# Performance work log

Hardware: AMD Instinct MI355X
Metric: run time of the kernel (lower is better)

The kernel has to match this reference:

```python
import jax, jax.numpy as jnp
import numpy as np

Q = 3
MAX_SHIFT = 4.0


def setup_inputs() -> dict:
    key = jax.random.key(0)
    k1, k2, k3, k4 = jax.random.split(key, 4)
    x = jax.random.normal(k1, (16, 64, 128, 128), jnp.float32)
    weight = jax.random.normal(k2, (64, 192, 3, 3), jnp.float32) * 0.05
    bias = jax.random.normal(k3, (64,), jnp.float32) * 0.05
    # shift_init='random': uniform in [-1, 1]; forward multiplies by max_shift
    shifts = jax.random.uniform(k4, (64, 2), jnp.float32, -1.0, 1.0)
    return {"x": x, "weight": weight, "bias": bias, "shifts": shifts}


def _shift_bilinear(x, shifts, max_shift):
    """Per-channel bilinear translation, matching affine_grid+grid_sample
    (align_corners=False, padding_mode='zeros').
    x: [N,C,H,W]; shifts: [C,2] with (sx, sy) in normalized units.
    Sample location for output (i,j) is (i + sy*max_shift, j + sx*max_shift)."""
    N, C, H, W = x.shape
    sx = shifts[:, 0] * max_shift  # pixels along width
    sy = shifts[:, 1] * max_shift  # pixels along height
    ys = jnp.arange(H, dtype=x.dtype)[None, :] + sy[:, None]  # [C,H]
    xs = jnp.arange(W, dtype=x.dtype)[None, :] + sx[:, None]  # [C,W]
    y0f = jnp.floor(ys); fy = ys - y0f; y0 = y0f.astype(jnp.int32); y1 = y0 + 1
    x0f = jnp.floor(xs); fx = xs - x0f; x0 = x0f.astype(jnp.int32); x1 = x0 + 1

    def gather(yi, xi):
        vy = (yi >= 0) & (yi < H)          # [C,H]
        vx = (xi >= 0) & (xi < W)          # [C,W]
        yc = jnp.clip(yi, 0, H - 1)
        xc = jnp.clip(xi, 0, W - 1)
        g = jnp.take_along_axis(x, yc[None, :, :, None], axis=2)
        g = jnp.take_along_axis(g, xc[None, :, None, :], axis=3)
        m = (vy[:, :, None] & vx[:, None, :]).astype(x.dtype)[None]
        return g * m

    w00 = ((1 - fy)[:, :, None] * (1 - fx)[:, None, :])[None]
    w01 = ((1 - fy)[:, :, None] * fx[:, None, :])[None]
    w10 = (fy[:, :, None] * (1 - fx)[:, None, :])[None]
    w11 = (fy[:, :, None] * fx[:, None, :])[None]
    return (w00 * gather(y0, x0) + w01 * gather(y0, x1)
            + w10 * gather(y1, x0) + w11 * gather(y1, x1))


def reference(x, weight, bias, shifts):
    # 1) per-channel learnless shift (grid_sample bilinear, zeros padding)
    xs = _shift_bilinear(x, shifts, MAX_SHIFT)
    # 2) Maclaurin power series: concat(x, x^2, ..., x^q) on channels -> [N, C*q, H, W]
    xq = jnp.concatenate([xs ** i for i in range(1, Q + 1)], axis=1)
    # 3) dense conv (groups=1), stride 1, padding 1
    out = jax.lax.conv_general_dilated(
        xq, weight, window_strides=(1, 1), padding=((1, 1), (1, 1)),
        dimension_numbers=("NCHW", "OIHW", "NCHW"))
    return out + bias[None, :, None, None]
```

## Files before the change

kernel.cpp:

```cpp
#include <hip/hip_runtime.h>
#include <hip/hip_bf16.h>
#include <math.h>

#define NB 16
#define C_IN 64
#define C_OUT 64
#define HH 128
#define WW 128
#define MAX_SHIFT 4.0f

typedef __attribute__((ext_vector_type(8))) short bf16x8;
typedef __attribute__((ext_vector_type(4))) float f32x4;
typedef __attribute__((ext_vector_type(4))) unsigned int u32x4;

__device__ inline unsigned short bf16_rne(float f) {
    unsigned u = __builtin_bit_cast(unsigned, f);
    u += 0x7fffu + ((u >> 16) & 1u);
    return (unsigned short)(u >> 16);
}
__device__ inline unsigned pack_bf16x2(float lo, float hi) {
    unsigned ul = __builtin_bit_cast(unsigned, lo);
    unsigned uh = __builtin_bit_cast(unsigned, hi);
    ul += 0x7fffu + ((ul >> 16) & 1u);
    uh += 0x7fffu + ((uh >> 16) & 1u);
    return (ul >> 16) | (uh & 0xffff0000u);
}

#define CPAD 66

__global__ __launch_bounds__(256)
void shift_v(const float* __restrict__ x, const float* __restrict__ shifts,
             unsigned short* __restrict__ xv) {
    __shared__ unsigned short row[64 * CPAD];
    __shared__ float s_fx[C_IN], s_fy[C_IN];
    __shared__ int s_dx[C_IN], s_dy[C_IN];

    int b = blockIdx.x;
    int wh = b & 1;
    int h  = (b >> 1) & 127;
    int n  = b >> 8;
    int tid = threadIdx.x;
    int wv = tid >> 6;
    int l  = tid & 63;

    if (tid < C_IN) {
        float sx = shifts[2 * tid] * MAX_SHIFT;
        float sy = shifts[2 * tid + 1] * MAX_SHIFT;
        float fx0 = floorf(sx), fy0 = floorf(sy);
        s_dx[tid] = (int)fx0; s_dy[tid] = (int)fy0;
        s_fx[tid] = sx - fx0;  s_fy[tid] = sy - fy0;
    }
    __syncthreads();

    const float* xn = x + (size_t)n * (C_IN * HH * WW);
    int w = wh * 64 + l;
    unsigned short* rw = row + l * CPAD;

    #pragma unroll 4
    for (int it = 0; it < 16; ++it) {
        int c = it * 4 + wv;
        int dx = s_dx[c], dy = s_dy[c];
        float fx = s_fx[c], fy = s_fy[c];
        const float* xp = xn + (size_t)c * (HH * WW);
        int y0 = h + dy, y1 = y0 + 1;
        bool vy0 = ((unsigned)y0 < (unsigned)HH);
        bool vy1 = ((unsigned)y1 < (unsigned)HH);
        const float* r0 = xp + y0 * WW;
        const float* r1 = xp + y1 * WW;

        int x0 = w + dx, x1 = x0 + 1;
        bool vx0 = ((unsigned)x0 < (unsigned)WW);
        bool vx1 = ((unsigned)x1 < (unsigned)WW);
        float v00 = (vy0 && vx0) ? r0[x0] : 0.f;
        float v01 = (vy0 && vx1) ? r0[x1] : 0.f;
        float v10 = (vy1 && vx0) ? r1[x0] : 0.f;
        float v11 = (vy1 && vx1) ? r1[x1] : 0.f;
        float v = (1.f - fy) * ((1.f - fx) * v00 + fx * v01)
                + fy * ((1.f - fx) * v10 + fx * v11);
        rw[c] = bf16_rne(v);
    }
    __syncthreads();

    const unsigned* rp = (const unsigned*)row;
    unsigned* dst = (unsigned*)xv + ((size_t)((n * HH + h) * WW) + wh * 64) * 32;
    #pragma unroll
    for (int itw = 0; itw < 8; ++itw) {
        int o32 = itw * 256 + tid;
        int wl = o32 >> 5;
        int c4 = o32 & 31;
        dst[o32] = rp[wl * (CPAD / 2) + c4];
    }
}

__global__ void prep_w3(const float* __restrict__ w, unsigned short* __restrict__ wbuf) {
    int id = blockIdx.x * 256 + threadIdx.x;
    int e = id & 7;
    int l = (id >> 3) & 63;
    int f = id >> 9;
    int mf = f & 3;
    int f2 = f >> 2;
    int kb = f2 % 6;
    int t  = f2 / 6;
    int cg = kb / 3;
    int p  = kb - cg * 3;
    int cl = (l >> 4) * 8 + e;
    int co = mf * 16 + (l & 15);
    wbuf[id] = bf16_rne(w[(co * 192 + p * 64 + cg * 32 + cl) * 9 + t]);
}

__global__ __launch_bounds__(256, 2)
void conv2d(const unsigned short* __restrict__ xv,
            const unsigned short* __restrict__ wbuf,
            const float* __restrict__ bias,
            float* __restrict__ out) {
    __shared__ unsigned short tile[324 * 44];

    int bid = blockIdx.x;
    int wg = (bid & 7) * 128 + (bid >> 3);
    int n  = wg >> 6;
    int t6 = wg & 63;
    int i0 = (t6 >> 3) * 16;
    int j0 = (t6 & 7) * 16;

    int tid = threadIdx.x;
    int l  = tid & 63;
    int wv = tid >> 6;
    int lm = l & 15;
    int lg = l >> 4;

    f32x4 acc[4][4];
    #pragma unroll
    for (int mf = 0; mf < 4; ++mf) {
        #pragma unroll
        for (int r = 0; r < 4; ++r) {
            float bv = bias[mf * 16 + lg * 4 + r];
            #pragma unroll
            for (int nf = 0; nf < 4; ++nf) acc[mf][nf][r] = bv;
        }
    }

    const unsigned short* xn = xv + (size_t)n * (HH * WW * 64);

    #pragma unroll 1
    for (int kb = 0; kb < 6; ++kb) {
        int cg = kb / 3;
        int p  = kb - cg * 3;
        __syncthreads();
        #pragma unroll
        for (int it = 0; it < 6; ++it) {
            int item = it * 256 + tid;
            if (item < 1296) {
                int px = item >> 2, sub = item & 3;
                int rr = px / 18;
                int cc = px - rr * 18;
                int gi = i0 - 1 + rr, gj = j0 - 1 + cc;
                u32x4 dv = {0, 0, 0, 0};
                if ((unsigned)gi < (unsigned)HH && (unsigned)gj < (unsigned)WW)
                    dv = *(const u32x4*)(xn + ((size_t)gi * WW + gj) * 64 + cg * 32 + sub * 8);
                u32x4 ov;
                if (p == 0) {
                    ov = dv;
                } else {
                    #pragma unroll
                    for (int q = 0; q < 4; ++q) {
                        unsigned u = dv[q];
                        float f0 = __builtin_bit_cast(float, u << 16);
                        float f1 = __builtin_bit_cast(float, u & 0xffff0000u);
                        float r0 = f0 * f0, r1 = f1 * f1;
                        if (p == 2) { r0 *= f0; r1 *= f1; }
                        ov[q] = pack_bf16x2(r0, r1);
                    }
                }
                *(u32x4*)((char*)tile + px * 88 + sub * 16) = ov;
            }
        }
        __syncthreads();

        bf16x8 Af[4];
        #pragma unroll
        for (int mf = 0; mf < 4; ++mf)
            Af[mf] = *(const bf16x8*)(wbuf + (size_t)((0 * 6 + kb) * 4 + mf) * 512 + l * 8);

        #pragma unroll 1
        for (int t = 0; t < 9; ++t) {
            bf16x8 Afn[4];
            int tn = (t < 8) ? t + 1 : t;
            #pragma unroll
            for (int mf = 0; mf < 4; ++mf)
                Afn[mf] = *(const bf16x8*)(wbuf + (size_t)((tn * 6 + kb) * 4 + mf) * 512 + l * 8);

            int ky = t / 3, kx = t - ky * 3;
            #pragma unroll
            for (int nf = 0; nf < 4; ++nf) {
                int off = ((wv * 4 + nf + ky) * 18 + (lm + kx)) * 88 + lg * 16;
                bf16x8 bfrag = *(const bf16x8*)((const char*)tile + off);
                #pragma unroll
                for (int mf = 0; mf < 4; ++mf)
                    acc[mf][nf] = __builtin_amdgcn_mfma_f32_16x16x32_bf16(Af[mf], bfrag, acc[mf][nf], 0, 0, 0);
            }
            #pragma unroll
            for (int mf = 0; mf < 4; ++mf) Af[mf] = Afn[mf];
        }
    }

    #pragma unroll
    for (int mf = 0; mf < 4; ++mf) {
        #pragma unroll
        for (int nf = 0; nf < 4; ++nf) {
            int rowi = i0 + wv * 4 + nf;
            int col = j0 + lm;
            #pragma unroll
            for (int r = 0; r < 4; ++r) {
                int co = mf * 16 + lg * 4 + r;
                out[(((size_t)n * C_OUT + co) * HH + rowi) * WW + col] = acc[mf][nf][r];
            }
        }
    }
}

#define S_PX 100

__global__ __launch_bounds__(256, 2)
void conv_f(const float* __restrict__ x,
            const float* __restrict__ shifts,
            const unsigned short* __restrict__ wbuf,
            const float* __restrict__ bias,
            float* __restrict__ out) {
    __shared__ unsigned short tile[324 * S_PX];
    __shared__ float s_fx[C_IN], s_fy[C_IN];
    __shared__ int s_dx[C_IN], s_dy[C_IN];

    int bid = blockIdx.x;
    int wg = (bid & 7) * 128 + (bid >> 3);
    int n  = wg >> 6;
    int t6 = wg & 63;
    int i0 = (t6 >> 3) * 16;
    int j0 = (t6 & 7) * 16;

    int tid = threadIdx.x;
    int l  = tid & 63;
    int wv = tid >> 6;
    int lm = l & 15;
    int lg = l >> 4;

    if (tid < C_IN) {
        float sx = shifts[2 * tid] * MAX_SHIFT;
        float sy = shifts[2 * tid + 1] * MAX_SHIFT;
        float fx0 = floorf(sx), fy0 = floorf(sy);
        s_dx[tid] = (int)fx0; s_dy[tid] = (int)fy0;
        s_fx[tid] = sx - fx0;  s_fy[tid] = sy - fy0;
    }

    f32x4 acc[4][4];
    #pragma unroll
    for (int mf = 0; mf < 4; ++mf) {
        #pragma unroll
        for (int r = 0; r < 4; ++r) {
            float bv = bias[mf * 16 + lg * 4 + r];
            #pragma unroll
            for (int nf = 0; nf < 4; ++nf) acc[mf][nf][r] = bv;
        }
    }

    const float* xn = x + (size_t)n * (C_IN * HH * WW);

    #pragma unroll 1
    for (int cg = 0; cg < 2; ++cg) {
        __syncthreads();
        #pragma unroll 2
        for (int it = 0; it < 21; ++it) {
            int item = it * 256 + tid;
            if (item < 5184) {
                int cl  = item / 162;
                int rem = item - cl * 162;
                int rp  = rem / 18;
                int cc  = rem - rp * 18;
                int c   = cg * 32 + cl;
                int dx = s_dx[c], dy = s_dy[c];
                float fx = s_fx[c], fy = s_fy[c];
                const float* xp = xn + (size_t)c * (HH * WW);

                int gj  = j0 - 1 + cc;
                int xx0 = gj + dx, xx1 = xx0 + 1;
                bool vx0 = ((unsigned)xx0 < (unsigned)WW);
                bool vx1 = ((unsigned)xx1 < (unsigned)WW);
                int gi0 = i0 - 1 + rp * 2;
                int y0  = gi0 + dy;
                bool vyA = ((unsigned)y0 < (unsigned)HH);
                bool vyB = ((unsigned)(y0 + 1) < (unsigned)HH);
                bool vyC = ((unsigned)(y0 + 2) < (unsigned)HH);
                const float* rA = xp + y0 * WW;
                const float* rB = rA + WW;
                const float* rC = rB + WW;
                float m0 = (vyA && vx0) ? rA[xx0] : 0.f;
                float m1 = (vyA && vx1) ? rA[xx1] : 0.f;
                float m2 = (vyB && vx0) ? rB[xx0] : 0.f;
                float m3 = (vyB && vx1) ? rB[xx1] : 0.f;
                float m4 = (vyC && vx0) ? rC[xx0] : 0.f;
                float m5 = (vyC && vx1) ? rC[xx1] : 0.f;
                float hA = (1.f - fx) * m0 + fx * m1;
                float hB = (1.f - fx) * m2 + fx * m3;
                float hC = (1.f - fx) * m4 + fx * m5;
                float vT = (1.f - fy) * hA + fy * hB;
                float vU = (1.f - fy) * hB + fy * hC;
                if (!((unsigned)gj < (unsigned)WW))        { vT = 0.f; vU = 0.f; }
                if (!((unsigned)gi0 < (unsigned)HH))       vT = 0.f;
                if (!((unsigned)(gi0 + 1) < (unsigned)HH)) vU = 0.f;

                float t2 = vT * vT, t3 = t2 * vT;
                float u2 = vU * vU, u3 = u2 * vU;
                unsigned short* recT = tile + (rp * 2 * 18 + cc) * S_PX;
                unsigned short* recU = recT + 18 * S_PX;
                recT[cl]      = bf16_rne(vT);
                recT[32 + cl] = bf16_rne(t2);
                recT[64 + cl] = bf16_rne(t3);
                recU[cl]      = bf16_rne(vU);
                recU[32 + cl] = bf16_rne(u2);
                recU[64 + cl] = bf16_rne(u3);
            }
        }
        __syncthreads();

        #pragma unroll 1
        for (int p = 0; p < 3; ++p) {
            int kb = cg * 3 + p;
            bf16x8 Af[4];
            #pragma unroll
            for (int mf = 0; mf < 4; ++mf)
                Af[mf] = *(const bf16x8*)(wbuf + (size_t)((0 * 6 + kb) * 4 + mf) * 512 + l * 8);

            #pragma unroll 1
            for (int t = 0; t < 9; ++t) {
                bf16x8 Afn[4];
                int tn = (t < 8) ? t + 1 : t;
                #pragma unroll
                for (int mf = 0; mf < 4; ++mf)
                    Afn[mf] = *(const bf16x8*)(wbuf + (size_t)((tn * 6 + kb) * 4 + mf) * 512 + l * 8);

                int ky = t / 3, kx = t - ky * 3;
                #pragma unroll
                for (int nf = 0; nf < 4; ++nf) {
                    int off = ((wv * 4 + nf + ky) * 18 + (lm + kx)) * 200 + p * 64 + lg * 16;
                    bf16x8 bfrag = *(const bf16x8*)((const char*)tile + off);
                    #pragma unroll
                    for (int mf = 0; mf < 4; ++mf)
                        acc[mf][nf] = __builtin_amdgcn_mfma_f32_16x16x32_bf16(Af[mf], bfrag, acc[mf][nf], 0, 0, 0);
                }
                #pragma unroll
                for (int mf = 0; mf < 4; ++mf) Af[mf] = Afn[mf];
            }
        }
    }

    #pragma unroll
    for (int mf = 0; mf < 4; ++mf) {
        #pragma unroll
        for (int nf = 0; nf < 4; ++nf) {
            int rowi = i0 + wv * 4 + nf;
            int col = j0 + lm;
            #pragma unroll
            for (int r = 0; r < 4; ++r) {
                int co = mf * 16 + lg * 4 + r;
                out[(((size_t)n * C_OUT + co) * HH + rowi) * WW + col] = acc[mf][nf][r];
            }
        }
    }
}

extern "C" void kernel_launch(void* const* d_in, const int* in_sizes, int n_in,
                              void* d_out, int out_size, void* d_ws, size_t ws_size,
                              hipStream_t stream) {
    (void)in_sizes; (void)n_in; (void)out_size;
    const float* x      = (const float*)d_in[0];
    const float* weight = (const float*)d_in[1];
    const float* bias   = (const float*)d_in[2];
    const float* shifts = (const float*)d_in[3];
    float* out = (float*)d_out;

    const size_t xv_elems = (size_t)NB * HH * WW * 64;
    const size_t need2 = xv_elems * 2 + 110592 * 2;

    if (ws_size >= need2) {
        unsigned short* xv   = (unsigned short*)d_ws;
        unsigned short* wbuf = xv + xv_elems;
        prep_w3<<<432, 256, 0, stream>>>(weight, wbuf);
        shift_v<<<NB * HH * 2, 256, 0, stream>>>(x, shifts, xv);
        conv2d<<<1024, 256, 0, stream>>>(xv, wbuf, bias, out);
    } else {
        unsigned short* wbuf = (unsigned short*)d_ws;
        prep_w3<<<432, 256, 0, stream>>>(weight, wbuf);
        conv_f<<<1024, 256, 0, stream>>>(x, shifts, wbuf, bias, out);
    }
}
```

Before: 114.2 us.

## Load input tile once per channel group, reuse for powers, raise occupancy

The conv kernel now loads each 32-channel input halo tile from global memory once into registers and builds the x, x^2 and x^3 LDS tiles from that copy, where before it reloaded the tile for every power. Launch bounds go from 2 to 4 blocks per CU. The weight software prefetch is removed to free registers in both conv kernels. In exchange, weight loads are no longer overlapped with the MFMAs, and the 24 prefetch registers plus the tighter register cap could cause spills.

```diff
diff --git a/kernel.cpp b/kernel.cpp
--- a/kernel.cpp
+++ b/kernel.cpp
@@ -108,8 +108,8 @@
     wbuf[id] = bf16_rne(w[(co * 192 + p * 64 + cg * 32 + cl) * 9 + t]);
 }
 
-__global__ __launch_bounds__(256, 2)
-void conv2d(const unsigned short* __restrict__ xv,
+__global__ __launch_bounds__(256, 4)
+void conv2e(const unsigned short* __restrict__ xv,
             const unsigned short* __restrict__ wbuf,
             const float* __restrict__ bias,
             float* __restrict__ out) {
@@ -141,65 +141,70 @@
 
     const unsigned short* xn = xv + (size_t)n * (HH * WW * 64);
 
+    u32x4 pf[6];
+
     #pragma unroll 1
-    for (int kb = 0; kb < 6; ++kb) {
-        int cg = kb / 3;
-        int p  = kb - cg * 3;
-        __syncthreads();
+    for (int cg = 0; cg < 2; ++cg) {
         #pragma unroll
         for (int it = 0; it < 6; ++it) {
             int item = it * 256 + tid;
+            u32x4 d = {0, 0, 0, 0};
             if (item < 1296) {
                 int px = item >> 2, sub = item & 3;
                 int rr = px / 18;
                 int cc = px - rr * 18;
                 int gi = i0 - 1 + rr, gj = j0 - 1 + cc;
-                u32x4 dv = {0, 0, 0, 0};
                 if ((unsigned)gi < (unsigned)HH && (unsigned)gj < (unsigned)WW)
-                    dv = *(const u32x4*)(xn + ((size_t)gi * WW + gj) * 64 + cg * 32 + sub * 8);
-                u32x4 ov;
-                if (p == 0) {
-                    ov = dv;
-                } else {
-                    #pragma unroll
-                    for (int q = 0; q < 4; ++q) {
-                        unsigned u = dv[q];
-                        float f0 = __builtin_bit_cast(float, u << 16);
-                        float f1 = __builtin_bit_cast(float, u & 0xffff0000u);
-                        float r0 = f0 * f0, r1 = f1 * f1;
-                        if (p == 2) { r0 *= f0; r1 *= f1; }
-                        ov[q] = pack_bf16x2(r0, r1);
+                    d = *(const u32x4*)(xn + ((size_t)gi * WW + gj) * 64 + cg * 32 + sub * 8);
+            }
+            pf[it] = d;
+        }
+
+        #pragma unroll 1
+        for (int p = 0; p < 3; ++p) {
+            int kb = cg * 3 + p;
+            __syncthreads();
+            #pragma unroll
+            for (int it = 0; it < 6; ++it) {
+                int item = it * 256 + tid;
+                if (item < 1296) {
+                    int px = item >> 2, sub = item & 3;
+                    u32x4 ov;
+                    if (p == 0) {
+                        ov = pf[it];
+                    } else {
+                        #pragma unroll
+                        for (int q = 0; q < 4; ++q) {
+                            unsigned u = pf[it][q];
+                            float f0 = __builtin_bit_cast(float, u << 16);
+                            float f1 = __builtin_bit_cast(float, u & 0xffff0000u);
+                            float r0 = f0 * f0, r1 = f1 * f1;
+                            if (p == 2) { r0 *= f0; r1 *= f1; }
+                            ov[q] = pack_bf16x2(r0, r1);
+                        }
                     }
+                    *(u32x4*)((char*)tile + px * 88 + sub * 16) = ov;
                 }
-                *(u32x4*)((char*)tile + px * 88 + sub * 16) = ov;
-            }
-        }
-        __syncthreads();
-
-        bf16x8 Af[4];
-        #pragma unroll
-        for (int mf = 0; mf < 4; ++mf)
-            Af[mf] = *(const bf16x8*)(wbuf + (size_t)((0 * 6 + kb) * 4 + mf) * 512 + l * 8);
-
-        #pragma unroll 1
-        for (int t = 0; t < 9; ++t) {
-            bf16x8 Afn[4];
-            int tn = (t < 8) ? t + 1 : t;
-            #pragma unroll
-            for (int mf = 0; mf < 4; ++mf)
-                Afn[mf] = *(const bf16x8*)(wbuf + (size_t)((tn * 6 + kb) * 4 + mf) * 512 + l * 8);
-
-            int ky = t / 3, kx = t - ky * 3;
-            #pragma unroll
-            for (int nf = 0; nf < 4; ++nf) {
-                int off = ((wv * 4 + nf + ky) * 18 + (lm + kx)) * 88 + lg * 16;
-                bf16x8 bfrag = *(const bf16x8*)((const char*)tile + off);
+            }
+            __syncthreads();
+
+            #pragma unroll 1
+            for (int t = 0; t < 9; ++t) {
+                bf16x8 Af[4];
                 #pragma unroll
                 for (int mf = 0; mf < 4; ++mf)
-                    acc[mf][nf] = __builtin_amdgcn_mfma_f32_16x16x32_bf16(Af[mf], bfrag, acc[mf][nf], 0, 0, 0);
-            }
-            #pragma unroll
-            for (int mf = 0; mf < 4; ++mf) Af[mf] = Afn[mf];
+                    Af[mf] = *(const bf16x8*)(wbuf + (size_t)((t * 6 + kb) * 4 + mf) * 512 + l * 8);
+
+                int ky = t / 3, kx = t - ky * 3;
+                #pragma unroll
+                for (int nf = 0; nf < 4; ++nf) {
+                    int off = ((wv * 4 + nf + ky) * 18 + (lm + kx)) * 88 + lg * 16;
+                    bf16x8 bfrag = *(const bf16x8*)((const char*)tile + off);
+                    #pragma unroll
+                    for (int mf = 0; mf < 4; ++mf)
+                        acc[mf][nf] = __builtin_amdgcn_mfma_f32_16x16x32_bf16(Af[mf], bfrag, acc[mf][nf], 0, 0, 0);
+                }
+            }
         }
     }
 
@@ -324,18 +329,12 @@
         #pragma unroll 1
         for (int p = 0; p < 3; ++p) {
             int kb = cg * 3 + p;
-            bf16x8 Af[4];
-            #pragma unroll
-            for (int mf = 0; mf < 4; ++mf)
-                Af[mf] = *(const bf16x8*)(wbuf + (size_t)((0 * 6 + kb) * 4 + mf) * 512 + l * 8);
-
             #pragma unroll 1
             for (int t = 0; t < 9; ++t) {
-                bf16x8 Afn[4];
-                int tn = (t < 8) ? t + 1 : t;
+                bf16x8 Af[4];
                 #pragma unroll
                 for (int mf = 0; mf < 4; ++mf)
-                    Afn[mf] = *(const bf16x8*)(wbuf + (size_t)((tn * 6 + kb) * 4 + mf) * 512 + l * 8);
+                    Af[mf] = *(const bf16x8*)(wbuf + (size_t)((t * 6 + kb) * 4 + mf) * 512 + l * 8);
 
                 int ky = t / 3, kx = t - ky * 3;
                 #pragma unroll
@@ -346,8 +345,6 @@
                     for (int mf = 0; mf < 4; ++mf)
                         acc[mf][nf] = __builtin_amdgcn_mfma_f32_16x16x32_bf16(Af[mf], bfrag, acc[mf][nf], 0, 0, 0);
                 }
-                #pragma unroll
-                for (int mf = 0; mf < 4; ++mf) Af[mf] = Afn[mf];
             }
         }
     }
@@ -385,7 +382,7 @@
         unsigned short* wbuf = xv + xv_elems;
         prep_w3<<<432, 256, 0, stream>>>(weight, wbuf);
         shift_v<<<NB * HH * 2, 256, 0, stream>>>(x, shifts, xv);
-        conv2d<<<1024, 256, 0, stream>>>(xv, wbuf, bias, out);
+        conv2e<<<1024, 256, 0, stream>>>(xv, wbuf, bias, out);
     } else {
         unsigned short* wbuf = (unsigned short*)d_ws;
         prep_w3<<<432, 256, 0, stream>>>(weight, wbuf);
```

After: 178.2 us. 1.56x slower.
